# Performance work log

Hardware: AMD Instinct MI355X
Metric: run time of the kernel (lower is better)

## Reference

```python
import jax, jax.numpy as jnp
import numpy as np

B = 16384       # batch of weight blocks
IN = 64         # input_size == e_dim
DENC = 512      # dim_encoder
NRES = 2        # n_resblock (weights shared, see ResidualStack [block]*n)
NE = 2048       # n_embeddings
P = 12          # basis vectors per block
BETA = 0.25
SCALE = 1.0
SHIFT = 0.0


def setup_inputs() -> dict:
    key = jax.random.key(0)
    ks = jax.random.split(key, 6)
    s = 0.02
    return {
        "x": jax.random.normal(ks[0], (B, IN), dtype=jnp.float32),
        "enc_w1": jax.random.normal(ks[1], (IN, DENC), dtype=jnp.float32) * s,
        "enc_b1": jnp.zeros((DENC,), jnp.float32),
        "res_w": jax.random.normal(ks[2], (DENC, DENC), dtype=jnp.float32) * s,
        "res_b": jnp.zeros((DENC,), jnp.float32),
        "res_g": jnp.ones((DENC,), jnp.float32),
        "res_beta": jnp.zeros((DENC,), jnp.float32),
        "enc_w2": jax.random.normal(ks[3], (DENC, IN * P), dtype=jnp.float32) * s,
        "enc_b2": jnp.zeros((IN * P,), jnp.float32),
        "emb": jax.random.uniform(ks[4], (NE, IN), jnp.float32, -1.0 / NE, 1.0 / NE),
    }


def _layer_norm(r, g, b):
    mu = jnp.mean(r, axis=-1, keepdims=True)
    var = jnp.mean((r - mu) ** 2, axis=-1, keepdims=True)
    return (r - mu) * jax.lax.rsqrt(var + 1e-5) * g + b


def reference(x, enc_w1, enc_b1, res_w, res_b, res_g, res_beta, enc_w2, enc_b2, emb):
    sg = jax.lax.stop_gradient
    x_shift = (x - SHIFT) / SCALE

    # encoder: Linear -> (shared ResBlock) x NRES -> Linear
    h = x_shift @ enc_w1 + enc_b1                      # (B, DENC)
    for _ in range(NRES):
        h = h + jax.nn.relu(_layer_norm(h @ res_w + res_b, res_g, res_beta))
    z = h @ enc_w2 + enc_b2                            # (B, P*IN)

    z_e = z.reshape(B, P, IN)
    zf = z_e.reshape(-1, IN)                           # (B*P, IN)

    # pairwise squared distances to codebook, argmin, gather
    d = (jnp.sum(zf ** 2, axis=1, keepdims=True)
         + jnp.sum(emb ** 2, axis=1)
         - 2.0 * zf @ emb.T)                           # (B*P, NE)
    idx = jnp.argmin(d, axis=1)                        # (B*P,)
    z_q = emb[idx].reshape(B, P, IN)

    loss = (jnp.mean((sg(z_q) - z_e) ** 2)
            + BETA * jnp.mean((z_q - sg(z_e)) ** 2))

    # straight-through estimator
    z_q = z_e + sg(z_q - z_e)

    counts = jnp.zeros((NE,), jnp.float32).at[idx].add(1.0) / idx.shape[0]
    perplexity = jnp.exp(-jnp.sum(counts * jnp.log(counts + 1e-10)))

    # pinv-based reconstruction: A (B, IN, P), coeff = pinv(A) @ x_shift
    A = jnp.transpose(z_q, (0, 2, 1))                  # (B, IN, P)
    coeff = jnp.matmul(jnp.linalg.pinv(A), x_shift[..., None])  # (B, P, 1)
    x_hat = jnp.matmul(A, coeff)[..., 0]               # (B, IN)
    x_hat = SCALE * x_hat + SHIFT

    return (loss, x_hat, perplexity, idx, coeff)
```

## Files before the change

kernel.cpp:

```cpp
#include <hip/hip_runtime.h>
#include <math.h>

#define B_    16384
#define IN_   64
#define DENC_ 512
#define NE_   2048
#define P_    12
#define ROWS_ 196608
#define BETA_ 0.25

#define XHAT_OFF 1
#define PERP_OFF 1048577
#define IDXF_OFF 1048578
#define COEF_OFF 1245186

typedef __bf16 bf16x8 __attribute__((ext_vector_type(8)));
typedef float  f32x16 __attribute__((ext_vector_type(16)));

__device__ __forceinline__ void split3(float v, __bf16& h, __bf16& m, __bf16& l) {
    h = (__bf16)v;
    float r1 = v - (float)h;
    m = (__bf16)r1;
    float r2 = r1 - (float)m;
    l = (__bf16)r2;
}

__device__ __forceinline__ void gload_lds16(const void* g, void* l) {
    __builtin_amdgcn_global_load_lds((const __attribute__((address_space(1))) void*)g,
                                     (__attribute__((address_space(3))) void*)l, 16, 0, 0);
}

__global__ void k_wsplit(const float* __restrict__ W,
                         __bf16* __restrict__ Wh, __bf16* __restrict__ Wm,
                         __bf16* __restrict__ Wl, int kshift, int N, int total) {
    int idx = blockIdx.x * 256 + threadIdx.x;
    if (idx < total) {
        int n = idx >> kshift;
        int k = idx & ((1 << kshift) - 1);
        float v = W[(size_t)k * N + n];
        __bf16 h, m, l;
        split3(v, h, m, l);
        Wh[idx] = h; Wm[idx] = m; Wl[idx] = l;
    }
}

__global__ __launch_bounds__(256) void k_gemm_mfma(const float* __restrict__ A,
                                                   const __bf16* __restrict__ Bh,
                                                   const __bf16* __restrict__ Bm,
                                                   const __bf16* __restrict__ Bl,
                                                   const float* __restrict__ bias,
                                                   float* __restrict__ C,
                                                   int N, int K) {
    __shared__ __bf16 eS[2][3][64 * 64];

    const int tid = threadIdx.x;
    const int w = tid >> 6, lane = tid & 63;
    const int r0 = blockIdx.y * 128 + w * 32;
    const int n0 = blockIdx.x * 64;
    const int lrow = lane & 31;
    const int half = lane >> 5;

    const int cc0 = tid >> 3, qq = tid & 7;
    const int cc1 = cc0 + 32;
    const size_t off0 = (size_t)cc0 * K + (size_t)((qq ^ (cc0 & 7)) * 8);
    const size_t off1 = (size_t)cc1 * K + (size_t)((qq ^ (cc1 & 7)) * 8);
    const size_t nbase = (size_t)n0 * K;
    const int ld0 = w * 512;
    const int ld1 = 2048 + w * 512;

    f32x16 acc0, acc1;
#pragma unroll
    for (int i = 0; i < 16; ++i) { acc0[i] = 0.0f; acc1[i] = 0.0f; }

    {
        const size_t b = nbase;
        gload_lds16(Bh + b + off0, &eS[0][0][ld0]);
        gload_lds16(Bh + b + off1, &eS[0][0][ld1]);
        gload_lds16(Bm + b + off0, &eS[0][1][ld0]);
        gload_lds16(Bm + b + off1, &eS[0][1][ld1]);
        gload_lds16(Bl + b + off0, &eS[0][2][ld0]);
        gload_lds16(Bl + b + off1, &eS[0][2][ld1]);
    }

    const int nch = K >> 6;
    for (int ch = 0; ch < nch; ++ch) {
        const int cur = ch & 1;
        __syncthreads();

        if (ch + 1 < nch) {
            const int nxt = cur ^ 1;
            const size_t b = nbase + (size_t)(ch + 1) * 64;
            gload_lds16(Bh + b + off0, &eS[nxt][0][ld0]);
            gload_lds16(Bh + b + off1, &eS[nxt][0][ld1]);
            gload_lds16(Bm + b + off0, &eS[nxt][1][ld0]);
            gload_lds16(Bm + b + off1, &eS[nxt][1][ld1]);
            gload_lds16(Bl + b + off0, &eS[nxt][2][ld0]);
            gload_lds16(Bl + b + off1, &eS[nxt][2][ld1]);
        }

        bf16x8 ah[4], am[4], al[4];
        {
            const float* ar = A + (size_t)(r0 + lrow) * K + ch * 64 + half * 8;
#pragma unroll
            for (int kc = 0; kc < 4; ++kc) {
                float4 u0 = *(const float4*)(ar + kc * 16);
                float4 u1 = *(const float4*)(ar + kc * 16 + 4);
                float v[8] = {u0.x, u0.y, u0.z, u0.w, u1.x, u1.y, u1.z, u1.w};
#pragma unroll
                for (int j = 0; j < 8; ++j) {
                    __bf16 hh, mm, ll;
                    split3(v[j], hh, mm, ll);
                    ah[kc][j] = hh; am[kc][j] = mm; al[kc][j] = ll;
                }
            }
        }

#pragma unroll
        for (int kc = 0; kc < 4; ++kc) {
            const int q = kc * 2 + half;
            const int g = (q ^ (lrow & 7)) * 8;
            bf16x8 b0h = *(const bf16x8*)(&eS[cur][0][lrow * 64 + g]);
            bf16x8 b0m = *(const bf16x8*)(&eS[cur][1][lrow * 64 + g]);
            bf16x8 b0l = *(const bf16x8*)(&eS[cur][2][lrow * 64 + g]);
            bf16x8 b1h = *(const bf16x8*)(&eS[cur][0][(lrow + 32) * 64 + g]);
            bf16x8 b1m = *(const bf16x8*)(&eS[cur][1][(lrow + 32) * 64 + g]);
            bf16x8 b1l = *(const bf16x8*)(&eS[cur][2][(lrow + 32) * 64 + g]);

            acc0 = __builtin_amdgcn_mfma_f32_32x32x16_bf16(ah[kc], b0h, acc0, 0, 0, 0);
            acc1 = __builtin_amdgcn_mfma_f32_32x32x16_bf16(ah[kc], b1h, acc1, 0, 0, 0);
            acc0 = __builtin_amdgcn_mfma_f32_32x32x16_bf16(ah[kc], b0m, acc0, 0, 0, 0);
            acc1 = __builtin_amdgcn_mfma_f32_32x32x16_bf16(ah[kc], b1m, acc1, 0, 0, 0);
            acc0 = __builtin_amdgcn_mfma_f32_32x32x16_bf16(am[kc], b0h, acc0, 0, 0, 0);
            acc1 = __builtin_amdgcn_mfma_f32_32x32x16_bf16(am[kc], b1h, acc1, 0, 0, 0);
            acc0 = __builtin_amdgcn_mfma_f32_32x32x16_bf16(ah[kc], b0l, acc0, 0, 0, 0);
            acc1 = __builtin_amdgcn_mfma_f32_32x32x16_bf16(ah[kc], b1l, acc1, 0, 0, 0);
            acc0 = __builtin_amdgcn_mfma_f32_32x32x16_bf16(am[kc], b0m, acc0, 0, 0, 0);
            acc1 = __builtin_amdgcn_mfma_f32_32x32x16_bf16(am[kc], b1m, acc1, 0, 0, 0);
            acc0 = __builtin_amdgcn_mfma_f32_32x32x16_bf16(al[kc], b0h, acc0, 0, 0, 0);
            acc1 = __builtin_amdgcn_mfma_f32_32x32x16_bf16(al[kc], b1h, acc1, 0, 0, 0);
        }
    }

    const int col0 = n0 + lrow, col1 = col0 + 32;
    const float bv0 = bias[col0], bv1 = bias[col1];
#pragma unroll
    for (int r = 0; r < 16; ++r) {
        int row = r0 + (r & 3) + 8 * (r >> 2) + 4 * half;
        C[(size_t)row * N + col0] = acc0[r] + bv0;
        C[(size_t)row * N + col1] = acc1[r] + bv1;
    }
}

__global__ __launch_bounds__(256) void k_lnrelu(const float* __restrict__ t,
                                                float* __restrict__ h,
                                                const float* __restrict__ g,
                                                const float* __restrict__ beta) {
    const int tid = threadIdx.x;
    const int wv = tid >> 6, lane = tid & 63;
    const int row = blockIdx.x * 4 + wv;
    const float* tr = t + (size_t)row * DENC_;
    float* hr = h + (size_t)row * DENC_;

    float4 v0 = *(const float4*)(tr + lane * 4);
    float4 v1 = *(const float4*)(tr + 256 + lane * 4);

    float s = v0.x + v0.y + v0.z + v0.w + v1.x + v1.y + v1.z + v1.w;
#pragma unroll
    for (int m = 1; m < 64; m <<= 1) s += __shfl_xor(s, m);
    float mu = s / 512.0f;

    float d0x = v0.x - mu, d0y = v0.y - mu, d0z = v0.z - mu, d0w = v0.w - mu;
    float d1x = v1.x - mu, d1y = v1.y - mu, d1z = v1.z - mu, d1w = v1.w - mu;
    float vs = d0x * d0x + d0y * d0y + d0z * d0z + d0w * d0w +
               d1x * d1x + d1y * d1y + d1z * d1z + d1w * d1w;
#pragma unroll
    for (int m = 1; m < 64; m <<= 1) vs += __shfl_xor(vs, m);
    float var = vs / 512.0f;
    float rs = (float)(1.0 / sqrt((double)var + 1e-5));

    float4 g0 = *(const float4*)(g + lane * 4);
    float4 g1 = *(const float4*)(g + 256 + lane * 4);
    float4 b0 = *(const float4*)(beta + lane * 4);
    float4 b1 = *(const float4*)(beta + 256 + lane * 4);

    float4 h0 = *(float4*)(hr + lane * 4);
    float4 h1 = *(float4*)(hr + 256 + lane * 4);

    h0.x += fmaxf(d0x * rs * g0.x + b0.x, 0.0f);
    h0.y += fmaxf(d0y * rs * g0.y + b0.y, 0.0f);
    h0.z += fmaxf(d0z * rs * g0.z + b0.z, 0.0f);
    h0.w += fmaxf(d0w * rs * g0.w + b0.w, 0.0f);
    h1.x += fmaxf(d1x * rs * g1.x + b1.x, 0.0f);
    h1.y += fmaxf(d1y * rs * g1.y + b1.y, 0.0f);
    h1.z += fmaxf(d1z * rs * g1.z + b1.z, 0.0f);
    h1.w += fmaxf(d1w * rs * g1.w + b1.w, 0.0f);

    *(float4*)(hr + lane * 4) = h0;
    *(float4*)(hr + 256 + lane * 4) = h1;
}

__global__ __launch_bounds__(256) void k_esplit_fast(const float* __restrict__ emb,
                                                     __bf16* __restrict__ Ehi,
                                                     __bf16* __restrict__ Emid,
                                                     __bf16* __restrict__ Elo) {
    const int wv = threadIdx.x >> 6, lane = threadIdx.x & 63;
    const int c = blockIdx.x * 4 + wv;
    float v = emb[(size_t)c * 64 + lane];
    __bf16 h, m, l;
    split3(v, h, m, l);
    Ehi[(size_t)c * 64 + lane] = h;
    Emid[(size_t)c * 64 + lane] = m;
    Elo[(size_t)c * 64 + lane] = l;
}

__global__ void k_esq(const float* __restrict__ emb, float* __restrict__ se) {
    int t = blockIdx.x * 256 + threadIdx.x;
    if (t < NE_) {
        float s = 0.0f;
        for (int k = 0; k < 64; ++k) {
            float v = emb[(size_t)t * 64 + k];
            s += v * v;
        }
        se[t] = s;
    }
}

__global__ __launch_bounds__(256) void k_rowsq(const float* __restrict__ z,
                                               float* __restrict__ sz) {
    const int tid = threadIdx.x;
    const int row = blockIdx.x * 64 + (tid >> 2);
    const int part = tid & 3;
    const float4* zp = (const float4*)(z + (size_t)row * 64) + part * 4;
    float s = 0.0f;
#pragma unroll
    for (int i = 0; i < 4; ++i) {
        float4 v = zp[i];
        s += v.x * v.x + v.y * v.y + v.z * v.z + v.w * v.w;
    }
    s += __shfl_xor(s, 1);
    s += __shfl_xor(s, 2);
    if (part == 0) sz[row] = s;
}

__global__ __launch_bounds__(256) void k_distm(const float* __restrict__ z,
                                               const float* __restrict__ se,
                                               const float* __restrict__ sz,
                                               const __bf16* __restrict__ Ehi,
                                               const __bf16* __restrict__ Emid,
                                               const __bf16* __restrict__ Elo,
                                               int* __restrict__ idxw,
                                               float* __restrict__ idxf,
                                               float* __restrict__ lossacc,
                                               int* __restrict__ counts) {
    __shared__ __bf16 eS[2][3][64 * 64];

    const int tid = threadIdx.x;
    const int w = tid >> 6, lane = tid & 63;
    const int r0 = blockIdx.x * 128 + w * 32;
    const int lrow = lane & 31;
    const int half = lane >> 5;

    const int cc0 = tid >> 3, qq = tid & 7;
    const int cc1 = cc0 + 32;
    const int off0 = cc0 * 64 + (qq ^ (cc0 & 7)) * 8;
    const int off1 = cc1 * 64 + (qq ^ (cc1 & 7)) * 8;
    const int ld0 = w * 512;
    const int ld1 = 2048 + w * 512;

    bf16x8 ah[4], am[4], al[4];
    {
        const float* zr = z + (size_t)(r0 + lrow) * 64 + half * 8;
#pragma unroll
        for (int kc = 0; kc < 4; ++kc) {
            float4 u0 = *(const float4*)(zr + kc * 16);
            float4 u1 = *(const float4*)(zr + kc * 16 + 4);
            float v[8] = {u0.x, u0.y, u0.z, u0.w, u1.x, u1.y, u1.z, u1.w};
#pragma unroll
            for (int j = 0; j < 8; ++j) {
                __bf16 hh, mm, ll;
                split3(v[j], hh, mm, ll);
                ah[kc][j] = hh; am[kc][j] = mm; al[kc][j] = ll;
            }
        }
    }

    float szv[16];
#pragma unroll
    for (int r = 0; r < 16; ++r) {
        int rl = (r & 3) + 8 * (r >> 2) + 4 * half;
        szv[r] = sz[r0 + rl];
    }

    float bd[16];
    int bi[16];
#pragma unroll
    for (int r = 0; r < 16; ++r) { bd[r] = 1e30f; bi[r] = 0; }

    gload_lds16(Ehi + off0, &eS[0][0][ld0]);
    gload_lds16(Ehi + off1, &eS[0][0][ld1]);
    gload_lds16(Emid + off0, &eS[0][1][ld0]);
    gload_lds16(Emid + off1, &eS[0][1][ld1]);
    gload_lds16(Elo + off0, &eS[0][2][ld0]);
    gload_lds16(Elo + off1, &eS[0][2][ld1]);

    for (int ch = 0; ch < 32; ++ch) {
        const int cur = ch & 1;
        __syncthreads();

        if (ch + 1 < 32) {
            const int nxt = cur ^ 1;
            const int b = (ch + 1) * 4096;
            gload_lds16(Ehi + b + off0, &eS[nxt][0][ld0]);
            gload_lds16(Ehi + b + off1, &eS[nxt][0][ld1]);
            gload_lds16(Emid + b + off0, &eS[nxt][1][ld0]);
            gload_lds16(Emid + b + off1, &eS[nxt][1][ld1]);
            gload_lds16(Elo + b + off0, &eS[nxt][2][ld0]);
            gload_lds16(Elo + b + off1, &eS[nxt][2][ld1]);
        }

        f32x16 acc0, acc1;
#pragma unroll
        for (int i = 0; i < 16; ++i) { acc0[i] = 0.0f; acc1[i] = 0.0f; }

#pragma unroll
        for (int kc = 0; kc < 4; ++kc) {
            const int q = kc * 2 + half;
            const int g = (q ^ (lrow & 7)) * 8;
            bf16x8 b0h = *(const bf16x8*)(&eS[cur][0][lrow * 64 + g]);
            bf16x8 b0m = *(const bf16x8*)(&eS[cur][1][lrow * 64 + g]);
            bf16x8 b0l = *(const bf16x8*)(&eS[cur][2][lrow * 64 + g]);
            bf16x8 b1h = *(const bf16x8*)(&eS[cur][0][(lrow + 32) * 64 + g]);
            bf16x8 b1m = *(const bf16x8*)(&eS[cur][1][(lrow + 32) * 64 + g]);
            bf16x8 b1l = *(const bf16x8*)(&eS[cur][2][(lrow + 32) * 64 + g]);

            acc0 = __builtin_amdgcn_mfma_f32_32x32x16_bf16(ah[kc], b0h, acc0, 0, 0, 0);
            acc1 = __builtin_amdgcn_mfma_f32_32x32x16_bf16(ah[kc], b1h, acc1, 0, 0, 0);
            acc0 = __builtin_amdgcn_mfma_f32_32x32x16_bf16(ah[kc], b0m, acc0, 0, 0, 0);
            acc1 = __builtin_amdgcn_mfma_f32_32x32x16_bf16(ah[kc], b1m, acc1, 0, 0, 0);
            acc0 = __builtin_amdgcn_mfma_f32_32x32x16_bf16(am[kc], b0h, acc0, 0, 0, 0);
            acc1 = __builtin_amdgcn_mfma_f32_32x32x16_bf16(am[kc], b1h, acc1, 0, 0, 0);
            acc0 = __builtin_amdgcn_mfma_f32_32x32x16_bf16(ah[kc], b0l, acc0, 0, 0, 0);
            acc1 = __builtin_amdgcn_mfma_f32_32x32x16_bf16(ah[kc], b1l, acc1, 0, 0, 0);
            acc0 = __builtin_amdgcn_mfma_f32_32x32x16_bf16(am[kc], b0m, acc0, 0, 0, 0);
            acc1 = __builtin_amdgcn_mfma_f32_32x32x16_bf16(am[kc], b1m, acc1, 0, 0, 0);
            acc0 = __builtin_amdgcn_mfma_f32_32x32x16_bf16(al[kc], b0h, acc0, 0, 0, 0);
            acc1 = __builtin_amdgcn_mfma_f32_32x32x16_bf16(al[kc], b1h, acc1, 0, 0, 0);
        }

        const int c0 = ch * 64;
        const float se0 = se[c0 + lrow];
        const float se1 = se[c0 + lrow + 32];
        const int   ci0 = c0 + lrow, ci1 = c0 + lrow + 32;
#pragma unroll
        for (int r = 0; r < 16; ++r) {
            float d0 = fmaf(-2.0f, acc0[r], szv[r] + se0);
            if (d0 < bd[r]) { bd[r] = d0; bi[r] = ci0; }
            float d1 = fmaf(-2.0f, acc1[r], szv[r] + se1);
            if (d1 < bd[r]) { bd[r] = d1; bi[r] = ci1; }
        }
    }

#pragma unroll
    for (int r = 0; r < 16; ++r) {
        float d = bd[r];
        int i = bi[r];
#pragma unroll
        for (int off = 1; off < 32; off <<= 1) {
            float od = __shfl_xor(d, off);
            int oi = __shfl_xor(i, off);
            if (od < d || (od == d && oi < i)) { d = od; i = oi; }
        }
        bd[r] = d; bi[r] = i;
    }

    if (lrow == 0) {
        float lsum = 0.0f;
#pragma unroll
        for (int r = 0; r < 16; ++r) {
            int rl = (r & 3) + 8 * (r >> 2) + 4 * half;
            int row = r0 + rl;
            idxw[row] = bi[r];
            idxf[row] = (float)bi[r];
            lsum += bd[r];
            atomicAdd(&counts[bi[r]], 1);
        }
        atomicAdd(lossacc, lsum);
    }
}

__global__ __launch_bounds__(256) void k_lossperp(const float* __restrict__ lossacc,
                                                  const int* __restrict__ counts,
                                                  float* __restrict__ out) {
    __shared__ double red[256];
    const int tid = threadIdx.x;

    double hsum = 0.0;
    for (int i = tid; i < NE_; i += 256) {
        float p = (float)counts[i] / 196608.0f;
        float lg = logf(p + 1e-10f);
        hsum += (double)(p * lg);
    }
    red[tid] = hsum;
    __syncthreads();
    for (int off = 128; off > 0; off >>= 1) {
        if (tid < off) red[tid] += red[tid + off];
        __syncthreads();
    }
    if (tid == 0) {
        out[PERP_OFF] = (float)exp(-red[0]);
        out[0] = (float)((double)lossacc[0] * (1.0 + BETA_) / ((double)ROWS_ * IN_));
    }
}

__global__ __launch_bounds__(256) void k_pinv(const float* __restrict__ xin,
                                              const float* __restrict__ emb,
                                              const int* __restrict__ idxw,
                                              float* __restrict__ coeff,
                                              float* __restrict__ xhat) {
    __shared__ float aS[4][12][65];
    __shared__ float xS[4][64];
    __shared__ double GS[4][12][12];
    __shared__ double bS[4][12];
    __shared__ double uS[4][12];
    __shared__ float cS[4][12];

    const int tid = threadIdx.x;
    const int wv = tid >> 6, lane = tid & 63;
    const int b = blockIdx.x * 4 + wv;

    int my = 0;
    if (lane < 12) my = idxw[(size_t)b * 12 + lane];
    int id[12];
#pragma unroll
    for (int p = 0; p < 12; ++p) id[p] = __shfl(my, p);

    int rep = lane, mcnt = 1;
    if (lane < 12) {
        rep = -1;
        mcnt = 0;
        for (int q = 0; q < 12; ++q) {
            if (id[q] == id[lane]) {
                if (rep < 0) rep = q;
                mcnt++;
            }
        }
    }

#pragma unroll
    for (int p = 0; p < 12; ++p) aS[wv][p][lane] = emb[(size_t)id[p] * 64 + lane];
    xS[wv][lane] = xin[(size_t)b * 64 + lane];
    __syncthreads();

    for (int item = lane; item < 90; item += 64) {
        if (item < 78) {
            int j = 0, k = 0, c = item;
            for (j = 0; j < 12; ++j) {
                int cnt = 12 - j;
                if (c < cnt) { k = j + c; break; }
                c -= cnt;
            }
            double s = 0.0;
            for (int t = 0; t < 64; ++t) s += (double)aS[wv][j][t] * (double)aS[wv][k][t];
            GS[wv][j][k] = s;
            GS[wv][k][j] = s;
        } else {
            int j = item - 78;
            double s = 0.0;
            for (int t = 0; t < 64; ++t) s += (double)aS[wv][j][t] * (double)xS[wv][t];
            bS[wv][j] = s;
        }
    }
    __syncthreads();

    if (lane == 0) {
        for (int p = 0; p < 12; ++p) {
            int rp = -1;
            for (int q = 0; q < 12; ++q) {
                if (id[q] == id[p]) { rp = q; break; }
            }
            if (rp != p) {
                for (int q = 0; q < 12; ++q) {
                    GS[wv][p][q] = 0.0;
                    GS[wv][q][p] = 0.0;
                }
                GS[wv][p][p] = 1.0;
                bS[wv][p] = 0.0;
            }
        }
    }
    __syncthreads();

    for (int j = 0; j < 12; ++j) {
        if (lane == j) {
            double s = GS[wv][j][j];
            for (int k = 0; k < j; ++k) {
                double l = GS[wv][j][k];
                s -= l * l;
            }
            GS[wv][j][j] = sqrt(fmax(s, 1e-30));
        }
        __syncthreads();
        if (lane > j && lane < 12) {
            double s = GS[wv][lane][j];
            for (int k = 0; k < j; ++k) s -= GS[wv][lane][k] * GS[wv][j][k];
            GS[wv][lane][j] = s / GS[wv][j][j];
        }
        __syncthreads();
    }

    if (lane == 0) {
        double y[12];
        for (int i = 0; i < 12; ++i) {
            double s = bS[wv][i];
            for (int k = 0; k < i; ++k) s -= GS[wv][i][k] * y[k];
            y[i] = s / GS[wv][i][i];
        }
        for (int i = 11; i >= 0; --i) {
            double s = y[i];
            for (int k = i + 1; k < 12; ++k) s -= GS[wv][k][i] * uS[wv][k];
            uS[wv][i] = s / GS[wv][i][i];
        }
    }
    __syncthreads();

    if (lane < 12) {
        double c = uS[wv][rep] / (double)mcnt;
        coeff[(size_t)b * 12 + lane] = (float)c;
        cS[wv][lane] = (float)c;
    }
    __syncthreads();

    float s = 0.0f;
#pragma unroll
    for (int p = 0; p < 12; ++p) s += aS[wv][p][lane] * cS[wv][p];
    xhat[(size_t)b * 64 + lane] = s;
}


extern "C" void kernel_launch(void* const* d_in, const int* in_sizes, int n_in,
                              void* d_out, int out_size, void* d_ws, size_t ws_size,
                              hipStream_t stream) {
    const float* x        = (const float*)d_in[0];
    const float* enc_w1   = (const float*)d_in[1];
    const float* enc_b1   = (const float*)d_in[2];
    const float* res_w    = (const float*)d_in[3];
    const float* res_b    = (const float*)d_in[4];
    const float* res_g    = (const float*)d_in[5];
    const float* res_beta = (const float*)d_in[6];
    const float* enc_w2   = (const float*)d_in[7];
    const float* enc_b2   = (const float*)d_in[8];
    const float* emb      = (const float*)d_in[9];

    float* out = (float*)d_out;

    float* h  = (float*)d_ws;
    float* tz = h + (size_t)B_ * DENC_;
    float* se    = h;
    float* sz    = h + 2048;
    int*   idxw  = (int*)(h + 2048 + (size_t)ROWS_);
    int*   cnts  = (int*)(h + 2048 + 2 * (size_t)ROWS_);
    float* lossacc = (float*)(cnts + NE_);
    __bf16* Ehi  = (__bf16*)(h + 2048 + 2 * (size_t)ROWS_ + 2048 + 16);
    __bf16* Emid = Ehi + (size_t)NE_ * 64;
    __bf16* Elo  = Emid + (size_t)NE_ * 64;
    __bf16* W1h = (__bf16*)(tz + (size_t)B_ * 768);
    __bf16* W1m = W1h + (size_t)DENC_ * IN_;
    __bf16* W1l = W1m + (size_t)DENC_ * IN_;
    __bf16* Wrh = W1l + (size_t)DENC_ * IN_;
    __bf16* Wrm = Wrh + (size_t)DENC_ * DENC_;
    __bf16* Wrl = Wrm + (size_t)DENC_ * DENC_;
    __bf16* W2h = Wrl + (size_t)DENC_ * DENC_;
    __bf16* W2m = W2h + (size_t)768 * DENC_;
    __bf16* W2l = W2m + (size_t)768 * DENC_;

    float* t = tz;
    float* z = tz;

    k_wsplit<<<(DENC_ * IN_ + 255) / 256, 256, 0, stream>>>(enc_w1, W1h, W1m, W1l, 6, DENC_, DENC_ * IN_);
    k_wsplit<<<(DENC_ * DENC_ + 255) / 256, 256, 0, stream>>>(res_w, Wrh, Wrm, Wrl, 9, DENC_, DENC_ * DENC_);
    k_wsplit<<<(768 * DENC_ + 255) / 256, 256, 0, stream>>>(enc_w2, W2h, W2m, W2l, 9, 768, 768 * DENC_);

    k_gemm_mfma<<<dim3(DENC_ / 64, B_ / 128), 256, 0, stream>>>(x, W1h, W1m, W1l, enc_b1, h, DENC_, IN_);
    for (int r = 0; r < 2; ++r) {
        k_gemm_mfma<<<dim3(DENC_ / 64, B_ / 128), 256, 0, stream>>>(h, Wrh, Wrm, Wrl, res_b, t, DENC_, DENC_);
        k_lnrelu<<<B_ / 4, 256, 0, stream>>>(t, h, res_g, res_beta);
    }
    k_gemm_mfma<<<dim3(768 / 64, B_ / 128), 256, 0, stream>>>(h, W2h, W2m, W2l, enc_b2, z, 768, DENC_);

    hipMemsetAsync(cnts, 0, (NE_ + 16) * sizeof(int), stream);
    k_esplit_fast<<<NE_ / 4, 256, 0, stream>>>(emb, Ehi, Emid, Elo);
    k_esq<<<NE_ / 256, 256, 0, stream>>>(emb, se);
    k_rowsq<<<ROWS_ / 64, 256, 0, stream>>>(z, sz);
    k_distm<<<ROWS_ / 128, 256, 0, stream>>>(z, se, sz, Ehi, Emid, Elo,
                                             idxw, out + IDXF_OFF, lossacc, cnts);
    k_lossperp<<<1, 256, 0, stream>>>(lossacc, cnts, out);
    k_pinv<<<B_ / 4, 256, 0, stream>>>(x, emb, idxw, out + COEF_OFF, out + XHAT_OFF);
}
```

Baseline: 773.8 us.

## Double GEMM row tile per wave and parallelize pinv triangular solves

```diff
diff --git a/kernel.cpp b/kernel.cpp
--- a/kernel.cpp
+++ b/kernel.cpp
@@ -44,18 +44,18 @@
     }
 }
 
-__global__ __launch_bounds__(256) void k_gemm_mfma(const float* __restrict__ A,
-                                                   const __bf16* __restrict__ Bh,
-                                                   const __bf16* __restrict__ Bm,
-                                                   const __bf16* __restrict__ Bl,
-                                                   const float* __restrict__ bias,
-                                                   float* __restrict__ C,
-                                                   int N, int K) {
+__global__ __launch_bounds__(256, 2) void k_gemm_mfma(const float* __restrict__ A,
+                                                      const __bf16* __restrict__ Bh,
+                                                      const __bf16* __restrict__ Bm,
+                                                      const __bf16* __restrict__ Bl,
+                                                      const float* __restrict__ bias,
+                                                      float* __restrict__ C,
+                                                      int N, int K) {
     __shared__ __bf16 eS[2][3][64 * 64];
 
     const int tid = threadIdx.x;
     const int w = tid >> 6, lane = tid & 63;
-    const int r0 = blockIdx.y * 128 + w * 32;
+    const int r0 = blockIdx.y * 256 + w * 64;
     const int n0 = blockIdx.x * 64;
     const int lrow = lane & 31;
     const int half = lane >> 5;
@@ -68,9 +68,9 @@
     const int ld0 = w * 512;
     const int ld1 = 2048 + w * 512;
 
-    f32x16 acc0, acc1;
-#pragma unroll
-    for (int i = 0; i < 16; ++i) { acc0[i] = 0.0f; acc1[i] = 0.0f; }
+    f32x16 acc00, acc01, acc10, acc11;
+#pragma unroll
+    for (int i = 0; i < 16; ++i) { acc00[i] = 0.0f; acc01[i] = 0.0f; acc10[i] = 0.0f; acc11[i] = 0.0f; }
 
     {
         const size_t b = nbase;
@@ -98,22 +98,249 @@
             gload_lds16(Bl + b + off1, &eS[nxt][2][ld1]);
         }
 
-        bf16x8 ah[4], am[4], al[4];
+        bf16x8 ah0[4], am0[4], al0[4], ah1[4], am1[4], al1[4];
         {
-            const float* ar = A + (size_t)(r0 + lrow) * K + ch * 64 + half * 8;
+            const float* ar0 = A + (size_t)(r0 + lrow) * K + ch * 64 + half * 8;
+            const float* ar1 = ar0 + (size_t)32 * K;
 #pragma unroll
             for (int kc = 0; kc < 4; ++kc) {
-                float4 u0 = *(const float4*)(ar + kc * 16);
-                float4 u1 = *(const float4*)(ar + kc * 16 + 4);
-                float v[8] = {u0.x, u0.y, u0.z, u0.w, u1.x, u1.y, u1.z, u1.w};
+                float4 u0 = *(const float4*)(ar0 + kc * 16);
+                float4 u1 = *(const float4*)(ar0 + kc * 16 + 4);
+                float va[8] = {u0.x, u0.y, u0.z, u0.w, u1.x, u1.y, u1.z, u1.w};
+                float4 t0 = *(const float4*)(ar1 + kc * 16);
+                float4 t1 = *(const float4*)(ar1 + kc * 16 + 4);
+                float vb[8] = {t0.x, t0.y, t0.z, t0.w, t1.x, t1.y, t1.z, t1.w};
 #pragma unroll
                 for (int j = 0; j < 8; ++j) {
                     __bf16 hh, mm, ll;
-                    split3(v[j], hh, mm, ll);
-                    ah[kc][j] = hh; am[kc][j] = mm; al[kc][j] = ll;
+                    split3(va[j], hh, mm, ll);
+                    ah0[kc][j] = hh; am0[kc][j] = mm; al0[kc][j] = ll;
+                    split3(vb[j], hh, mm, ll);
+                    ah1[kc][j] = hh; am1[kc][j] = mm; al1[kc][j] = ll;
                 }
             }
         }
+
+#pragma unroll
+        for (int kc = 0; kc < 4; ++kc) {
+            const int q = kc * 2 + half;
+            const int g = (q ^ (lrow & 7)) * 8;
+            bf16x8 b0h = *(const bf16x8*)(&eS[cur][0][lrow * 64 + g]);
+            bf16x8 b0m = *(const bf16x8*)(&eS[cur][1][lrow * 64 + g]);
+            bf16x8 b0l = *(const bf16x8*)(&eS[cur][2][lrow * 64 + g]);
+            bf16x8 b1h = *(const bf16x8*)(&eS[cur][0][(lrow + 32) * 64 + g]);
+            bf16x8 b1m = *(const bf16x8*)(&eS[cur][1][(lrow + 32) * 64 + g]);
+            bf16x8 b1l = *(const bf16x8*)(&eS[cur][2][(lrow + 32) * 64 + g]);
+
+            acc00 = __builtin_amdgcn_mfma_f32_32x32x16_bf16(ah0[kc], b0h, acc00, 0, 0, 0);
+            acc01 = __builtin_amdgcn_mfma_f32_32x32x16_bf16(ah0[kc], b1h, acc01, 0, 0, 0);
+            acc10 = __builtin_amdgcn_mfma_f32_32x32x16_bf16(ah1[kc], b0h, acc10, 0, 0, 0);
+            acc11 = __builtin_amdgcn_mfma_f32_32x32x16_bf16(ah1[kc], b1h, acc11, 0, 0, 0);
+            acc00 = __builtin_amdgcn_mfma_f32_32x32x16_bf16(ah0[kc], b0m, acc00, 0, 0, 0);
+            acc01 = __builtin_amdgcn_mfma_f32_32x32x16_bf16(ah0[kc], b1m, acc01, 0, 0, 0);
+            acc10 = __builtin_amdgcn_mfma_f32_32x32x16_bf16(ah1[kc], b0m, acc10, 0, 0, 0);
+            acc11 = __builtin_amdgcn_mfma_f32_32x32x16_bf16(ah1[kc], b1m, acc11, 0, 0, 0);
+            acc00 = __builtin_amdgcn_mfma_f32_32x32x16_bf16(am0[kc], b0h, acc00, 0, 0, 0);
+            acc01 = __builtin_amdgcn_mfma_f32_32x32x16_bf16(am0[kc], b1h, acc01, 0, 0, 0);
+            acc10 = __builtin_amdgcn_mfma_f32_32x32x16_bf16(am1[kc], b0h, acc10, 0, 0, 0);
+            acc11 = __builtin_amdgcn_mfma_f32_32x32x16_bf16(am1[kc], b1h, acc11, 0, 0, 0);
+            acc00 = __builtin_amdgcn_mfma_f32_32x32x16_bf16(ah0[kc], b0l, acc00, 0, 0, 0);
+            acc01 = __builtin_amdgcn_mfma_f32_32x32x16_bf16(ah0[kc], b1l, acc01, 0, 0, 0);
+            acc10 = __builtin_amdgcn_mfma_f32_32x32x16_bf16(ah1[kc], b0l, acc10, 0, 0, 0);
+            acc11 = __builtin_amdgcn_mfma_f32_32x32x16_bf16(ah1[kc], b1l, acc11, 0, 0, 0);
+            acc00 = __builtin_amdgcn_mfma_f32_32x32x16_bf16(am0[kc], b0m, acc00, 0, 0, 0);
+            acc01 = __builtin_amdgcn_mfma_f32_32x32x16_bf16(am0[kc], b1m, acc01, 0, 0, 0);
+            acc10 = __builtin_amdgcn_mfma_f32_32x32x16_bf16(am1[kc], b0m, acc10, 0, 0, 0);
+            acc11 = __builtin_amdgcn_mfma_f32_32x32x16_bf16(am1[kc], b1m, acc11, 0, 0, 0);
+            acc00 = __builtin_amdgcn_mfma_f32_32x32x16_bf16(al0[kc], b0h, acc00, 0, 0, 0);
+            acc01 = __builtin_amdgcn_mfma_f32_32x32x16_bf16(al0[kc], b1h, acc01, 0, 0, 0);
+            acc10 = __builtin_amdgcn_mfma_f32_32x32x16_bf16(al1[kc], b0h, acc10, 0, 0, 0);
+            acc11 = __builtin_amdgcn_mfma_f32_32x32x16_bf16(al1[kc], b1h, acc11, 0, 0, 0);
+        }
+    }
+
+    const int col0 = n0 + lrow, col1 = col0 + 32;
+    const float bv0 = bias[col0], bv1 = bias[col1];
+#pragma unroll
+    for (int r = 0; r < 16; ++r) {
+        int rr = (r & 3) + 8 * (r >> 2) + 4 * half;
+        C[(size_t)(r0 + rr) * N + col0] = acc00[r] + bv0;
+        C[(size_t)(r0 + rr) * N + col1] = acc01[r] + bv1;
+        C[(size_t)(r0 + 32 + rr) * N + col0] = acc10[r] + bv0;
+        C[(size_t)(r0 + 32 + rr) * N + col1] = acc11[r] + bv1;
+    }
+}
+
+__global__ __launch_bounds__(256) void k_lnrelu(const float* __restrict__ t,
+                                                float* __restrict__ h,
+                                                const float* __restrict__ g,
+                                                const float* __restrict__ beta) {
+    const int tid = threadIdx.x;
+    const int wv = tid >> 6, lane = tid & 63;
+    const int row = blockIdx.x * 4 + wv;
+    const float* tr = t + (size_t)row * DENC_;
+    float* hr = h + (size_t)row * DENC_;
+
+    float4 v0 = *(const float4*)(tr + lane * 4);
+    float4 v1 = *(const float4*)(tr + 256 + lane * 4);
+
+    float s = v0.x + v0.y + v0.z + v0.w + v1.x + v1.y + v1.z + v1.w;
+#pragma unroll
+    for (int m = 1; m < 64; m <<= 1) s += __shfl_xor(s, m);
+    float mu = s / 512.0f;
+
+    float d0x = v0.x - mu, d0y = v0.y - mu, d0z = v0.z - mu, d0w = v0.w - mu;
+    float d1x = v1.x - mu, d1y = v1.y - mu, d1z = v1.z - mu, d1w = v1.w - mu;
+    float vs = d0x * d0x + d0y * d0y + d0z * d0z + d0w * d0w +
+               d1x * d1x + d1y * d1y + d1z * d1z + d1w * d1w;
+#pragma unroll
+    for (int m = 1; m < 64; m <<= 1) vs += __shfl_xor(vs, m);
+    float var = vs / 512.0f;
+    float rs = (float)(1.0 / sqrt((double)var + 1e-5));
+
+    float4 g0 = *(const float4*)(g + lane * 4);
+    float4 g1 = *(const float4*)(g + 256 + lane * 4);
+    float4 b0 = *(const float4*)(beta + lane * 4);
+    float4 b1 = *(const float4*)(beta + 256 + lane * 4);
+
+    float4 h0 = *(float4*)(hr + lane * 4);
+    float4 h1 = *(float4*)(hr + 256 + lane * 4);
+
+    h0.x += fmaxf(d0x * rs * g0.x + b0.x, 0.0f);
+    h0.y += fmaxf(d0y * rs * g0.y + b0.y, 0.0f);
+    h0.z += fmaxf(d0z * rs * g0.z + b0.z, 0.0f);
+    h0.w += fmaxf(d0w * rs * g0.w + b0.w, 0.0f);
+    h1.x += fmaxf(d1x * rs * g1.x + b1.x, 0.0f);
+    h1.y += fmaxf(d1y * rs * g1.y + b1.y, 0.0f);
+    h1.z += fmaxf(d1z * rs * g1.z + b1.z, 0.0f);
+    h1.w += fmaxf(d1w * rs * g1.w + b1.w, 0.0f);
+
+    *(float4*)(hr + lane * 4) = h0;
+    *(float4*)(hr + 256 + lane * 4) = h1;
+}
+
+__global__ __launch_bounds__(256) void k_esplit_fast(const float* __restrict__ emb,
+                                                     __bf16* __restrict__ Ehi,
+                                                     __bf16* __restrict__ Emid,
+                                                     __bf16* __restrict__ Elo) {
+    const int wv = threadIdx.x >> 6, lane = threadIdx.x & 63;
+    const int c = blockIdx.x * 4 + wv;
+    float v = emb[(size_t)c * 64 + lane];
+    __bf16 h, m, l;
+    split3(v, h, m, l);
+    Ehi[(size_t)c * 64 + lane] = h;
+    Emid[(size_t)c * 64 + lane] = m;
+    Elo[(size_t)c * 64 + lane] = l;
+}
+
+__global__ void k_esq(const float* __restrict__ emb, float* __restrict__ se) {
+    int t = blockIdx.x * 256 + threadIdx.x;
+    if (t < NE_) {
+        float s = 0.0f;
+        for (int k = 0; k < 64; ++k) {
+            float v = emb[(size_t)t * 64 + k];
+            s += v * v;
+        }
+        se[t] = s;
+    }
+}
+
+__global__ __launch_bounds__(256) void k_rowsq(const float* __restrict__ z,
+                                               float* __restrict__ sz) {
+    const int tid = threadIdx.x;
+    const int row = blockIdx.x * 64 + (tid >> 2);
+    const int part = tid & 3;
+    const float4* zp = (const float4*)(z + (size_t)row * 64) + part * 4;
+    float s = 0.0f;
+#pragma unroll
+    for (int i = 0; i < 4; ++i) {
+        float4 v = zp[i];
+        s += v.x * v.x + v.y * v.y + v.z * v.z + v.w * v.w;
+    }
+    s += __shfl_xor(s, 1);
+    s += __shfl_xor(s, 2);
+    if (part == 0) sz[row] = s;
+}
+
+__global__ __launch_bounds__(256) void k_distm(const float* __restrict__ z,
+                                               const float* __restrict__ se,
+                                               const float* __restrict__ sz,
+                                               const __bf16* __restrict__ Ehi,
+                                               const __bf16* __restrict__ Emid,
+                                               const __bf16* __restrict__ Elo,
+                                               int* __restrict__ idxw,
+                                               float* __restrict__ idxf,
+                                               float* __restrict__ lossacc,
+                                               int* __restrict__ counts) {
+    __shared__ __bf16 eS[2][3][64 * 64];
+
+    const int tid = threadIdx.x;
+    const int w = tid >> 6, lane = tid & 63;
+    const int r0 = blockIdx.x * 128 + w * 32;
+    const int lrow = lane & 31;
+    const int half = lane >> 5;
+
+    const int cc0 = tid >> 3, qq = tid & 7;
+    const int cc1 = cc0 + 32;
+    const int off0 = cc0 * 64 + (qq ^ (cc0 & 7)) * 8;
+    const int off1 = cc1 * 64 + (qq ^ (cc1 & 7)) * 8;
+    const int ld0 = w * 512;
+    const int ld1 = 2048 + w * 512;
+
+    bf16x8 ah[4], am[4], al[4];
+    {
+        const float* zr = z + (size_t)(r0 + lrow) * 64 + half * 8;
+#pragma unroll
+        for (int kc = 0; kc < 4; ++kc) {
+            float4 u0 = *(const float4*)(zr + kc * 16);
+            float4 u1 = *(const float4*)(zr + kc * 16 + 4);
+            float v[8] = {u0.x, u0.y, u0.z, u0.w, u1.x, u1.y, u1.z, u1.w};
+#pragma unroll
+            for (int j = 0; j < 8; ++j) {
+                __bf16 hh, mm, ll;
+                split3(v[j], hh, mm, ll);
+                ah[kc][j] = hh; am[kc][j] = mm; al[kc][j] = ll;
+            }
+        }
+    }
+
+    float szv[16];
+#pragma unroll
+    for (int r = 0; r < 16; ++r) {
+        int rl = (r & 3) + 8 * (r >> 2) + 4 * half;
+        szv[r] = sz[r0 + rl];
+    }
+
+    float bd[16];
+    int bi[16];
+#pragma unroll
+    for (int r = 0; r < 16; ++r) { bd[r] = 1e30f; bi[r] = 0; }
+
+    gload_lds16(Ehi + off0, &eS[0][0][ld0]);
+    gload_lds16(Ehi + off1, &eS[0][0][ld1]);
+    gload_lds16(Emid + off0, &eS[0][1][ld0]);
+    gload_lds16(Emid + off1, &eS[0][1][ld1]);
+    gload_lds16(Elo + off0, &eS[0][2][ld0]);
+    gload_lds16(Elo + off1, &eS[0][2][ld1]);
+
+    for (int ch = 0; ch < 32; ++ch) {
+        const int cur = ch & 1;
+        __syncthreads();
+
+        if (ch + 1 < 32) {
+            const int nxt = cur ^ 1;
+            const int b = (ch + 1) * 4096;
+            gload_lds16(Ehi + b + off0, &eS[nxt][0][ld0]);
+            gload_lds16(Ehi + b + off1, &eS[nxt][0][ld1]);
+            gload_lds16(Emid + b + off0, &eS[nxt][1][ld0]);
+            gload_lds16(Emid + b + off1, &eS[nxt][1][ld1]);
+            gload_lds16(Elo + b + off0, &eS[nxt][2][ld0]);
+            gload_lds16(Elo + b + off1, &eS[nxt][2][ld1]);
+        }
+
+        f32x16 acc0, acc1;
+#pragma unroll
+        for (int i = 0; i < 16; ++i) { acc0[i] = 0.0f; acc1[i] = 0.0f; }
 
 #pragma unroll
         for (int kc = 0; kc < 4; ++kc) {
@@ -139,213 +366,6 @@
             acc0 = __builtin_amdgcn_mfma_f32_32x32x16_bf16(al[kc], b0h, acc0, 0, 0, 0);
             acc1 = __builtin_amdgcn_mfma_f32_32x32x16_bf16(al[kc], b1h, acc1, 0, 0, 0);
         }
-    }
-
-    const int col0 = n0 + lrow, col1 = col0 + 32;
-    const float bv0 = bias[col0], bv1 = bias[col1];
-#pragma unroll
-    for (int r = 0; r < 16; ++r) {
-        int row = r0 + (r & 3) + 8 * (r >> 2) + 4 * half;
-        C[(size_t)row * N + col0] = acc0[r] + bv0;
-        C[(size_t)row * N + col1] = acc1[r] + bv1;
-    }
-}
-
-__global__ __launch_bounds__(256) void k_lnrelu(const float* __restrict__ t,
-                                                float* __restrict__ h,
-                                                const float* __restrict__ g,
-                                                const float* __restrict__ beta) {
-    const int tid = threadIdx.x;
-    const int wv = tid >> 6, lane = tid & 63;
-    const int row = blockIdx.x * 4 + wv;
-    const float* tr = t + (size_t)row * DENC_;
-    float* hr = h + (size_t)row * DENC_;
-
-    float4 v0 = *(const float4*)(tr + lane * 4);
-    float4 v1 = *(const float4*)(tr + 256 + lane * 4);
-
-    float s = v0.x + v0.y + v0.z + v0.w + v1.x + v1.y + v1.z + v1.w;
-#pragma unroll
-    for (int m = 1; m < 64; m <<= 1) s += __shfl_xor(s, m);
-    float mu = s / 512.0f;
-
-    float d0x = v0.x - mu, d0y = v0.y - mu, d0z = v0.z - mu, d0w = v0.w - mu;
-    float d1x = v1.x - mu, d1y = v1.y - mu, d1z = v1.z - mu, d1w = v1.w - mu;
-    float vs = d0x * d0x + d0y * d0y + d0z * d0z + d0w * d0w +
-               d1x * d1x + d1y * d1y + d1z * d1z + d1w * d1w;
-#pragma unroll
-    for (int m = 1; m < 64; m <<= 1) vs += __shfl_xor(vs, m);
-    float var = vs / 512.0f;
-    float rs = (float)(1.0 / sqrt((double)var + 1e-5));
-
-    float4 g0 = *(const float4*)(g + lane * 4);
-    float4 g1 = *(const float4*)(g + 256 + lane * 4);
-    float4 b0 = *(const float4*)(beta + lane * 4);
-    float4 b1 = *(const float4*)(beta + 256 + lane * 4);
-
-    float4 h0 = *(float4*)(hr + lane * 4);
-    float4 h1 = *(float4*)(hr + 256 + lane * 4);
-
-    h0.x += fmaxf(d0x * rs * g0.x + b0.x, 0.0f);
-    h0.y += fmaxf(d0y * rs * g0.y + b0.y, 0.0f);
-    h0.z += fmaxf(d0z * rs * g0.z + b0.z, 0.0f);
-    h0.w += fmaxf(d0w * rs * g0.w + b0.w, 0.0f);
-    h1.x += fmaxf(d1x * rs * g1.x + b1.x, 0.0f);
-    h1.y += fmaxf(d1y * rs * g1.y + b1.y, 0.0f);
-    h1.z += fmaxf(d1z * rs * g1.z + b1.z, 0.0f);
-    h1.w += fmaxf(d1w * rs * g1.w + b1.w, 0.0f);
-
-    *(float4*)(hr + lane * 4) = h0;
-    *(float4*)(hr + 256 + lane * 4) = h1;
-}
-
-__global__ __launch_bounds__(256) void k_esplit_fast(const float* __restrict__ emb,
-                                                     __bf16* __restrict__ Ehi,
-                                                     __bf16* __restrict__ Emid,
-                                                     __bf16* __restrict__ Elo) {
-    const int wv = threadIdx.x >> 6, lane = threadIdx.x & 63;
-    const int c = blockIdx.x * 4 + wv;
-    float v = emb[(size_t)c * 64 + lane];
-    __bf16 h, m, l;
-    split3(v, h, m, l);
-    Ehi[(size_t)c * 64 + lane] = h;
-    Emid[(size_t)c * 64 + lane] = m;
-    Elo[(size_t)c * 64 + lane] = l;
-}
-
-__global__ void k_esq(const float* __restrict__ emb, float* __restrict__ se) {
-    int t = blockIdx.x * 256 + threadIdx.x;
-    if (t < NE_) {
-        float s = 0.0f;
-        for (int k = 0; k < 64; ++k) {
-            float v = emb[(size_t)t * 64 + k];
-            s += v * v;
-        }
-        se[t] = s;
-    }
-}
-
-__global__ __launch_bounds__(256) void k_rowsq(const float* __restrict__ z,
-                                               float* __restrict__ sz) {
-    const int tid = threadIdx.x;
-    const int row = blockIdx.x * 64 + (tid >> 2);
-    const int part = tid & 3;
-    const float4* zp = (const float4*)(z + (size_t)row * 64) + part * 4;
-    float s = 0.0f;
-#pragma unroll
-    for (int i = 0; i < 4; ++i) {
-        float4 v = zp[i];
-        s += v.x * v.x + v.y * v.y + v.z * v.z + v.w * v.w;
-    }
-    s += __shfl_xor(s, 1);
-    s += __shfl_xor(s, 2);
-    if (part == 0) sz[row] = s;
-}
-
-__global__ __launch_bounds__(256) void k_distm(const float* __restrict__ z,
-                                               const float* __restrict__ se,
-                                               const float* __restrict__ sz,
-                                               const __bf16* __restrict__ Ehi,
-                                               const __bf16* __restrict__ Emid,
-                                               const __bf16* __restrict__ Elo,
-                                               int* __restrict__ idxw,
-                                               float* __restrict__ idxf,
-                                               float* __restrict__ lossacc,
-                                               int* __restrict__ counts) {
-    __shared__ __bf16 eS[2][3][64 * 64];
-
-    const int tid = threadIdx.x;
-    const int w = tid >> 6, lane = tid & 63;
-    const int r0 = blockIdx.x * 128 + w * 32;
-    const int lrow = lane & 31;
-    const int half = lane >> 5;
-
-    const int cc0 = tid >> 3, qq = tid & 7;
-    const int cc1 = cc0 + 32;
-    const int off0 = cc0 * 64 + (qq ^ (cc0 & 7)) * 8;
-    const int off1 = cc1 * 64 + (qq ^ (cc1 & 7)) * 8;
-    const int ld0 = w * 512;
-    const int ld1 = 2048 + w * 512;
-
-    bf16x8 ah[4], am[4], al[4];
-    {
-        const float* zr = z + (size_t)(r0 + lrow) * 64 + half * 8;
-#pragma unroll
-        for (int kc = 0; kc < 4; ++kc) {
-            float4 u0 = *(const float4*)(zr + kc * 16);
-            float4 u1 = *(const float4*)(zr + kc * 16 + 4);
-            float v[8] = {u0.x, u0.y, u0.z, u0.w, u1.x, u1.y, u1.z, u1.w};
-#pragma unroll
-            for (int j = 0; j < 8; ++j) {
-                __bf16 hh, mm, ll;
-                split3(v[j], hh, mm, ll);
-                ah[kc][j] = hh; am[kc][j] = mm; al[kc][j] = ll;
-            }
-        }
-    }
-
-    float szv[16];
-#pragma unroll
-    for (int r = 0; r < 16; ++r) {
-        int rl = (r & 3) + 8 * (r >> 2) + 4 * half;
-        szv[r] = sz[r0 + rl];
-    }
-
-    float bd[16];
-    int bi[16];
-#pragma unroll
-    for (int r = 0; r < 16; ++r) { bd[r] = 1e30f; bi[r] = 0; }
-
-    gload_lds16(Ehi + off0, &eS[0][0][ld0]);
-    gload_lds16(Ehi + off1, &eS[0][0][ld1]);
-    gload_lds16(Emid + off0, &eS[0][1][ld0]);
-    gload_lds16(Emid + off1, &eS[0][1][ld1]);
-    gload_lds16(Elo + off0, &eS[0][2][ld0]);
-    gload_lds16(Elo + off1, &eS[0][2][ld1]);
-
-    for (int ch = 0; ch < 32; ++ch) {
-        const int cur = ch & 1;
-        __syncthreads();
-
-        if (ch + 1 < 32) {
-            const int nxt = cur ^ 1;
-            const int b = (ch + 1) * 4096;
-            gload_lds16(Ehi + b + off0, &eS[nxt][0][ld0]);
-            gload_lds16(Ehi + b + off1, &eS[nxt][0][ld1]);
-            gload_lds16(Emid + b + off0, &eS[nxt][1][ld0]);
-            gload_lds16(Emid + b + off1, &eS[nxt][1][ld1]);
-            gload_lds16(Elo + b + off0, &eS[nxt][2][ld0]);
-            gload_lds16(Elo + b + off1, &eS[nxt][2][ld1]);
-        }
-
-        f32x16 acc0, acc1;
-#pragma unroll
-        for (int i = 0; i < 16; ++i) { acc0[i] = 0.0f; acc1[i] = 0.0f; }
-
-#pragma unroll
-        for (int kc = 0; kc < 4; ++kc) {
-            const int q = kc * 2 + half;
-            const int g = (q ^ (lrow & 7)) * 8;
-            bf16x8 b0h = *(const bf16x8*)(&eS[cur][0][lrow * 64 + g]);
-            bf16x8 b0m = *(const bf16x8*)(&eS[cur][1][lrow * 64 + g]);
-            bf16x8 b0l = *(const bf16x8*)(&eS[cur][2][lrow * 64 + g]);
-            bf16x8 b1h = *(const bf16x8*)(&eS[cur][0][(lrow + 32) * 64 + g]);
-            bf16x8 b1m = *(const bf16x8*)(&eS[cur][1][(lrow + 32) * 64 + g]);
-            bf16x8 b1l = *(const bf16x8*)(&eS[cur][2][(lrow + 32) * 64 + g]);
-
-            acc0 = __builtin_amdgcn_mfma_f32_32x32x16_bf16(ah[kc], b0h, acc0, 0, 0, 0);
-            acc1 = __builtin_amdgcn_mfma_f32_32x32x16_bf16(ah[kc], b1h, acc1, 0, 0, 0);
-            acc0 = __builtin_amdgcn_mfma_f32_32x32x16_bf16(ah[kc], b0m, acc0, 0, 0, 0);
-            acc1 = __builtin_amdgcn_mfma_f32_32x32x16_bf16(ah[kc], b1m, acc1, 0, 0, 0);
-            acc0 = __builtin_amdgcn_mfma_f32_32x32x16_bf16(am[kc], b0h, acc0, 0, 0, 0);
-            acc1 = __builtin_amdgcn_mfma_f32_32x32x16_bf16(am[kc], b1h, acc1, 0, 0, 0);
-            acc0 = __builtin_amdgcn_mfma_f32_32x32x16_bf16(ah[kc], b0l, acc0, 0, 0, 0);
-            acc1 = __builtin_amdgcn_mfma_f32_32x32x16_bf16(ah[kc], b1l, acc1, 0, 0, 0);
-            acc0 = __builtin_amdgcn_mfma_f32_32x32x16_bf16(am[kc], b0m, acc0, 0, 0, 0);
-            acc1 = __builtin_amdgcn_mfma_f32_32x32x16_bf16(am[kc], b1m, acc1, 0, 0, 0);
-            acc0 = __builtin_amdgcn_mfma_f32_32x32x16_bf16(al[kc], b0h, acc0, 0, 0, 0);
-            acc1 = __builtin_amdgcn_mfma_f32_32x32x16_bf16(al[kc], b1h, acc1, 0, 0, 0);
-        }
 
         const int c0 = ch * 64;
         const float se0 = se[c0 + lrow];
@@ -412,21 +432,21 @@
     }
 }
 
-__global__ __launch_bounds__(256) void k_pinv(const float* __restrict__ xin,
-                                              const float* __restrict__ emb,
-                                              const int* __restrict__ idxw,
-                                              float* __restrict__ coeff,
-                                              float* __restrict__ xhat) {
-    __shared__ float aS[4][12][65];
-    __shared__ float xS[4][64];
-    __shared__ double GS[4][12][12];
-    __shared__ double bS[4][12];
-    __shared__ double uS[4][12];
-    __shared__ float cS[4][12];
-
-    const int tid = threadIdx.x;
-    const int wv = tid >> 6, lane = tid & 63;
-    const int b = blockIdx.x * 4 + wv;
+__global__ __launch_bounds__(64) void k_pinv(const float* __restrict__ xin,
+                                             const float* __restrict__ emb,
+                                             const int* __restrict__ idxw,
+                                             float* __restrict__ coeff,
+                                             float* __restrict__ xhat) {
+    __shared__ float aS[12][65];
+    __shared__ float xS[64];
+    __shared__ double GS[12][12];
+    __shared__ double bS[12];
+    __shared__ double yS[12];
+    __shared__ double uS[12];
+    __shared__ float cS[12];
+
+    const int lane = threadIdx.x;
+    const int b = blockIdx.x;
 
     int my = 0;
     if (lane < 12) my = idxw[(size_t)b * 12 + lane];
@@ -447,8 +467,8 @@
     }
 
 #pragma unroll
-    for (int p = 0; p < 12; ++p) aS[wv][p][lane] = emb[(size_t)id[p] * 64 + lane];
-    xS[wv][lane] = xin[(size_t)b * 64 + lane];
+    for (int p = 0; p < 12; ++p) aS[p][lane] = emb[(size_t)id[p] * 64 + lane];
+    xS[lane] = xin[(size_t)b * 64 + lane];
     __syncthreads();
 
     for (int item = lane; item < 90; item += 64) {
@@ -460,14 +480,14 @@
                 c -= cnt;
             }
             double s = 0.0;
-            for (int t = 0; t < 64; ++t) s += (double)aS[wv][j][t] * (double)aS[wv][k][t];
-            GS[wv][j][k] = s;
-            GS[wv][k][j] = s;
+            for (int t = 0; t < 64; ++t) s += (double)aS[j][t] * (double)aS[k][t];
+            GS[j][k] = s;
+            GS[k][j] = s;
         } else {
             int j = item - 78;
             double s = 0.0;
-            for (int t = 0; t < 64; ++t) s += (double)aS[wv][j][t] * (double)xS[wv][t];
-            bS[wv][j] = s;
+            for (int t = 0; t < 64; ++t) s += (double)aS[j][t] * (double)xS[t];
+            bS[j] = s;
         }
     }
     __syncthreads();
@@ -480,11 +500,11 @@
             }
             if (rp != p) {
                 for (int q = 0; q < 12; ++q) {
-                    GS[wv][p][q] = 0.0;
-                    GS[wv][q][p] = 0.0;
+                    GS[p][q] = 0.0;
+                    GS[q][p] = 0.0;
                 }
-                GS[wv][p][p] = 1.0;
-                bS[wv][p] = 0.0;
+                GS[p][p] = 1.0;
+                bS[p] = 0.0;
             }
         }
     }
@@ -492,48 +512,49 @@
 
     for (int j = 0; j < 12; ++j) {
         if (lane == j) {
-            double s = GS[wv][j][j];
+            double s = GS[j][j];
             for (int k = 0; k < j; ++k) {
-                double l = GS[wv][j][k];
+                double l = GS[j][k];
                 s -= l * l;
             }
-            GS[wv][j][j] = sqrt(fmax(s, 1e-30));
+            GS[j][j] = sqrt(fmax(s, 1e-30));
         }
         __syncthreads();
         if (lane > j && lane < 12) {
-            double s = GS[wv][lane][j];
-            for (int k = 0; k < j; ++k) s -= GS[wv][lane][k] * GS[wv][j][k];
-            GS[wv][lane][j] = s / GS[wv][j][j];
+            double s = GS[lane][j];
+            for (int k = 0; k < j; ++k) s -= GS[lane][k] * GS[j][k];
+            GS[lane][j] = s / GS[j][j];
         }
         __syncthreads();
     }
 
-    if (lane == 0) {
-        double y[12];
-        for (int i = 0; i < 12; ++i) {
-            double s = bS[wv][i];
-            for (int k = 0; k < i; ++k) s -= GS[wv][i][k] * y[k];
-            y[i] = s / GS[wv][i][i];
-        }
-        for (int i = 11; i >= 0; --i) {
-            double s = y[i];
-            for (int k = i + 1; k < 12; ++k) s -= GS[wv][k][i] * uS[wv][k];
-            uS[wv][i] = s / GS[wv][i][i];
-        }
+    double s = (lane < 12) ? bS[lane] : 0.0;
+    for (int k = 0; k < 12; ++k) {
+        if (lane == k) yS[k] = s / GS[k][k];
+        __syncthreads();
+        double yk = yS[k];
+        if (lane > k && lane < 12) s -= GS[lane][k] * yk;
+    }
+    double tacc = 0.0;
+    for (int k = 11; k >= 0; --k) {
+        if (lane == k) uS[k] = (yS[k] - tacc) / GS[k][k];
+        __syncthreads();
+        double uk = uS[k];
+        if (lane < k) tacc += GS[k][lane] * uk;
     }
     __syncthreads();
 
     if (lane < 12) {
-        double c = uS[wv][rep] / (double)mcnt;
+        double c = uS[rep] / (double)mcnt;
         coeff[(size_t)b * 12 + lane] = (float)c;
-        cS[wv][lane] = (float)c;
+        cS[lane] = (float)c;
     }
     __syncthreads();
 
-    float s = 0.0f;
-#pragma unroll
-    for (int p = 0; p < 12; ++p) s += aS[wv][p][lane] * cS[wv][p];
-    xhat[(size_t)b * 64 + lane] = s;
+    float sx = 0.0f;
+#pragma unroll
+    for (int p = 0; p < 12; ++p) sx += aS[p][lane] * cS[p];
+    xhat[(size_t)b * 64 + lane] = sx;
 }
 
 
@@ -580,12 +601,12 @@
     k_wsplit<<<(DENC_ * DENC_ + 255) / 256, 256, 0, stream>>>(res_w, Wrh, Wrm, Wrl, 9, DENC_, DENC_ * DENC_);
     k_wsplit<<<(768 * DENC_ + 255) / 256, 256, 0, stream>>>(enc_w2, W2h, W2m, W2l, 9, 768, 768 * DENC_);
 
-    k_gemm_mfma<<<dim3(DENC_ / 64, B_ / 128), 256, 0, stream>>>(x, W1h, W1m, W1l, enc_b1, h, DENC_, IN_);
+    k_gemm_mfma<<<dim3(DENC_ / 64, B_ / 256), 256, 0, stream>>>(x, W1h, W1m, W1l, enc_b1, h, DENC_, IN_);
     for (int r = 0; r < 2; ++r) {
-        k_gemm_mfma<<<dim3(DENC_ / 64, B_ / 128), 256, 0, stream>>>(h, Wrh, Wrm, Wrl, res_b, t, DENC_, DENC_);
+        k_gemm_mfma<<<dim3(DENC_ / 64, B_ / 256), 256, 0, stream>>>(h, Wrh, Wrm, Wrl, res_b, t, DENC_, DENC_);
         k_lnrelu<<<B_ / 4, 256, 0, stream>>>(t, h, res_g, res_beta);
     }
-    k_gemm_mfma<<<dim3(768 / 64, B_ / 128), 256, 0, stream>>>(h, W2h, W2m, W2l, enc_b2, z, 768, DENC_);
+    k_gemm_mfma<<<dim3(768 / 64, B_ / 256), 256, 0, stream>>>(h, W2h, W2m, W2l, enc_b2, z, 768, DENC_);
 
     hipMemsetAsync(cnts, 0, (NE_ + 16) * sizeof(int), stream);
     k_esplit_fast<<<NE_ / 4, 256, 0, stream>>>(emb, Ehi, Emid, Elo);
@@ -594,5 +615,5 @@
     k_distm<<<ROWS_ / 128, 256, 0, stream>>>(z, se, sz, Ehi, Emid, Elo,
                                              idxw, out + IDXF_OFF, lossacc, cnts);
     k_lossperp<<<1, 256, 0, stream>>>(lossacc, cnts, out);
-    k_pinv<<<B_ / 4, 256, 0, stream>>>(x, emb, idxw, out + COEF_OFF, out + XHAT_OFF);
-}
+    k_pinv<<<B_, 64, 0, stream>>>(x, emb, idxw, out + COEF_OFF, out + XHAT_OFF);
+}
```

Result: faster. 744.3 us (-3.8%).
